# Kernel tuning notes

Hardware: AMD Instinct MI355X
Metric: run time of the kernel (lower is better)

Reference implementation:

```python
import jax, jax.numpy as jnp
import numpy as np

DIM = 512
INNER = 512  # heads*dim_head = 8*64
SCALE = 64 ** -0.5  # dim_head^{-0.5}, applied to BOTH q and k as in the source


def setup_inputs() -> dict:
    key = jax.random.key(0)
    k1, k2, k3, k4 = jax.random.split(key, 4)
    x = jax.random.normal(k1, (8, 2048, DIM), dtype=jnp.float32)
    Wqkv = jax.random.normal(k2, (DIM, 3 * INNER), dtype=jnp.float32) * (DIM ** -0.5)
    Wout = jax.random.normal(k3, (INNER, DIM), dtype=jnp.float32) * (INNER ** -0.5)
    bout = jax.random.normal(k4, (DIM,), dtype=jnp.float32) * 0.01
    return {"x": x, "Wqkv": Wqkv, "Wout": Wout, "bout": bout}


def reference(x, Wqkv, Wout, bout):
    # fused QKV projection (no bias)
    qkv = jnp.einsum("bnd,de->bne", x, Wqkv)
    q, k, v = jnp.split(qkv, 3, axis=-1)
    # note: source scales BOTH q and k by dim_head^{-0.5}
    scores = jnp.einsum("bnd,bmd->bnm", q * SCALE, k * SCALE)  # [B,N,N]
    attn = jax.nn.softmax(scores, axis=-1)
    out = jnp.einsum("bnm,bmd->bnd", attn, v)
    # residual add, then output projection (dropout=0.0 -> identity)
    return jnp.einsum("bnd,de->bne", out + x, Wout) + bout
```

## Files before the change

### kernel.cpp

```cpp
#include <hip/hip_runtime.h>
#include <hip/hip_bf16.h>


typedef __attribute__((ext_vector_type(8))) short bf16x8;
typedef __attribute__((ext_vector_type(4))) float f32x4;

__device__ __forceinline__ unsigned short f2bf(float f) {
  unsigned u = __builtin_bit_cast(unsigned, f);
  u += 0x7fffu + ((u >> 16) & 1u);
  return (unsigned short)(u >> 16);
}
__device__ __forceinline__ float bf2f(unsigned short h) {
  unsigned u = ((unsigned)h) << 16;
  return __builtin_bit_cast(float, u);
}

__device__ __forceinline__ void async16(const unsigned short* g, unsigned short* l) {
  __builtin_amdgcn_global_load_lds(
      (const __attribute__((address_space(1))) unsigned int*)g,
      (__attribute__((address_space(3))) unsigned int*)l, 16, 0, 0);
}

__global__ __launch_bounds__(256) void prep_x(const float* __restrict__ X,
                                              unsigned short* __restrict__ XB) {
  const size_t base = ((size_t)blockIdx.x * 256 + threadIdx.x) * 16;
  f32x4 a0 = *(const f32x4*)&X[base];
  f32x4 a1 = *(const f32x4*)&X[base + 4];
  f32x4 a2 = *(const f32x4*)&X[base + 8];
  f32x4 a3 = *(const f32x4*)&X[base + 12];
  bf16x8 o0, o1;
#pragma unroll
  for (int j = 0; j < 4; ++j) {
    o0[j] = (short)f2bf(a0[j]);
    o0[4 + j] = (short)f2bf(a1[j]);
    o1[j] = (short)f2bf(a2[j]);
    o1[4 + j] = (short)f2bf(a3[j]);
  }
  *(bf16x8*)&XB[base] = o0;
  *(bf16x8*)&XB[base + 8] = o1;
}

__global__ __launch_bounds__(256) void prep_w(const float* __restrict__ W,
                                              unsigned short* __restrict__ WT) {
  const int t = threadIdx.x;
  const int c0 = blockIdx.x * 128 + (t & 15) * 8;
  const int k0 = blockIdx.y * 128 + (t >> 4) * 8;
  float r[8][8];
#pragma unroll
  for (int j = 0; j < 8; ++j) {
    f32x4 lo = *(const f32x4*)&W[(size_t)(k0 + j) * 1536 + c0];
    f32x4 hi = *(const f32x4*)&W[(size_t)(k0 + j) * 1536 + c0 + 4];
#pragma unroll
    for (int q = 0; q < 4; ++q) {
      r[j][q] = lo[q];
      r[j][4 + q] = hi[q];
    }
  }
#pragma unroll
  for (int i = 0; i < 8; ++i) {
    const float scl = (c0 + i < 1024) ? 0.125f : 1.0f;
    bf16x8 o;
#pragma unroll
    for (int j = 0; j < 8; ++j) o[j] = (short)f2bf(r[j][i] * scl);
    *(bf16x8*)&WT[(size_t)(c0 + i) * 512 + k0] = o;
  }
}

__global__ __launch_bounds__(256) void transpose_wout(const float* __restrict__ W,
                                                      unsigned short* __restrict__ WT) {
  const int t = threadIdx.x;
  const int c0 = blockIdx.x * 128 + (t & 15) * 8;
  const int k0 = blockIdx.y * 128 + (t >> 4) * 8;
  float r[8][8];
#pragma unroll
  for (int j = 0; j < 8; ++j) {
    f32x4 lo = *(const f32x4*)&W[(size_t)(k0 + j) * 512 + c0];
    f32x4 hi = *(const f32x4*)&W[(size_t)(k0 + j) * 512 + c0 + 4];
#pragma unroll
    for (int q = 0; q < 4; ++q) {
      r[j][q] = lo[q];
      r[j][4 + q] = hi[q];
    }
  }
#pragma unroll
  for (int i = 0; i < 8; ++i) {
    bf16x8 o;
#pragma unroll
    for (int j = 0; j < 8; ++j) o[j] = (short)f2bf(r[j][i]);
    *(bf16x8*)&WT[(size_t)(c0 + i) * 512 + k0] = o;
  }
}

__global__ __launch_bounds__(256) void transpose_v(const unsigned short* __restrict__ QKV,
                                                   unsigned short* __restrict__ VT) {
  const int t = threadIdx.x;
  const int m0 = blockIdx.x * 128 + (t & 15) * 8;
  const int d0 = blockIdx.y * 128 + (t >> 4) * 8;
  bf16x8 r[8];
#pragma unroll
  for (int j = 0; j < 8; ++j)
    r[j] = *(const bf16x8*)&QKV[(size_t)(m0 + j) * 1536 + 1024 + d0];
#pragma unroll
  for (int i = 0; i < 8; ++i) {
    bf16x8 o;
#pragma unroll
    for (int j = 0; j < 8; ++j) o[j] = r[j][i];
    *(bf16x8*)&VT[(size_t)(d0 + i) * 16384 + m0] = o;
  }
}


#define GEMM97_VARS                                            \
  const int tid = threadIdx.x;                                 \
  const int wave = tid >> 6, lane = tid & 63;                  \
  const int wr = wave >> 1, wc = wave & 1;                     \
  const int lg = lane >> 4, ll = lane & 15;                    \
  const int kk = lg * 8;                                       \
  const int srow = wave * 32 + (lane >> 2);                    \
  const int scol = (lane & 3) * 8;

#define GEMM97_BODY(AG, ASTR, BG, BSTR, KDIM)                                            \
  __shared__ __align__(16) unsigned short Asm[4096];                                     \
  __shared__ __align__(16) unsigned short Bsm[4096];                                     \
  GEMM97_VARS                                                                            \
  f32x4 acc[4][4];                                                                       \
  _Pragma("unroll") for (int i = 0; i < 4; ++i) _Pragma("unroll") for (int j = 0; j < 4; \
                                                                       ++j) acc[i][j] =  \
      (f32x4){0.f, 0.f, 0.f, 0.f};                                                       \
  for (int kt = 0; kt < KDIM; kt += 32) {                                                \
    async16(&AG[(size_t)srow * ASTR + kt + scol], &Asm[wave * 1024]);                    \
    async16(&AG[(size_t)(srow + 16) * ASTR + kt + scol], &Asm[wave * 1024 + 512]);       \
    async16(&BG[(size_t)srow * BSTR + kt + scol], &Bsm[wave * 1024]);                    \
    async16(&BG[(size_t)(srow + 16) * BSTR + kt + scol], &Bsm[wave * 1024 + 512]);       \
    __syncthreads();                                                                     \
    bf16x8 af[4], bfr[4];                                                                \
    _Pragma("unroll") for (int ai = 0; ai < 4; ++ai) af[ai] =                            \
        *(const bf16x8*)&Asm[(wr * 64 + ai * 16 + ll) * 32 + kk];                        \
    _Pragma("unroll") for (int bj = 0; bj < 4; ++bj) bfr[bj] =                           \
        *(const bf16x8*)&Bsm[(wc * 64 + bj * 16 + ll) * 32 + kk];                        \
    _Pragma("unroll") for (int ai = 0; ai < 4; ++ai) _Pragma("unroll") for (int bj = 0;  \
                                                                            bj < 4;      \
                                                                            ++bj)        \
        acc[ai][bj] =                                                                    \
        __builtin_amdgcn_mfma_f32_16x16x32_bf16(af[ai], bfr[bj], acc[ai][bj], 0, 0, 0);  \
    __syncthreads();                                                                     \
  }

__global__ __launch_bounds__(256, 3) void gemm_qkv97(const unsigned short* __restrict__ XB,
                                                     const unsigned short* __restrict__ WT,
                                                     unsigned short* __restrict__ QKV) {
  const int bid = blockIdx.x;
  const int qt = bid / 12, nt = bid - qt * 12;
  const unsigned short* Ag = XB + (size_t)(qt * 128) * 512;
  const unsigned short* Bg = WT + (size_t)(nt * 128) * 512;
  GEMM97_BODY(Ag, 512, Bg, 512, 512)
#pragma unroll
  for (int ai = 0; ai < 4; ++ai)
#pragma unroll
    for (int bj = 0; bj < 4; ++bj) {
      const int col = nt * 128 + wc * 64 + bj * 16 + ll;
#pragma unroll
      for (int r = 0; r < 4; ++r) {
        const int row = qt * 128 + wr * 64 + ai * 16 + lg * 4 + r;
        QKV[(size_t)row * 1536 + col] = f2bf(acc[ai][bj][r]);
      }
    }
}

__global__ __launch_bounds__(256, 3) void sgemm97(const unsigned short* __restrict__ QKV,
                                                  unsigned short* __restrict__ S,
                                                  float* __restrict__ part) {
  const int bid = blockIdx.x;
  const int b = bid & 7;
  const int idx = bid >> 3;
  const int kvt = idx & 15, qt = idx >> 4;
  const unsigned short* Ag = QKV + ((size_t)b * 2048 + qt * 128) * 1536;
  const unsigned short* Bg = QKV + ((size_t)b * 2048 + kvt * 128) * 1536 + 512;
  GEMM97_BODY(Ag, 1536, Bg, 1536, 512)

#pragma unroll
  for (int ai = 0; ai < 4; ++ai)
#pragma unroll
    for (int bj = 0; bj < 4; ++bj)
#pragma unroll
      for (int r = 0; r < 4; ++r) acc[ai][bj][r] = __expf(acc[ai][bj][r]);

#pragma unroll
  for (int ai = 0; ai < 4; ++ai)
#pragma unroll
    for (int r = 0; r < 4; ++r) {
      float se = (acc[ai][0][r] + acc[ai][1][r]) + (acc[ai][2][r] + acc[ai][3][r]);
      se += __shfl_xor(se, 1);
      se += __shfl_xor(se, 2);
      se += __shfl_xor(se, 4);
      se += __shfl_xor(se, 8);
      if (ll == 0) {
        const size_t rowg = (size_t)b * 2048 + qt * 128 + wr * 64 + ai * 16 + lg * 4 + r;
        part[rowg * 32 + kvt * 2 + wc] = se;
      }
    }

  unsigned short* Sg = S + (size_t)b * 2048 * 2048;
#pragma unroll
  for (int ai = 0; ai < 4; ++ai)
#pragma unroll
    for (int bj = 0; bj < 4; ++bj) {
      const int col = kvt * 128 + wc * 64 + bj * 16 + ll;
#pragma unroll
      for (int r = 0; r < 4; ++r) {
        const int row = qt * 128 + wr * 64 + ai * 16 + lg * 4 + r;
        Sg[(size_t)row * 2048 + col] = f2bf(acc[ai][bj][r]);
      }
    }
}

__global__ __launch_bounds__(256) void combine_l(const float* __restrict__ part,
                                                 float* __restrict__ invl) {
  const int row = blockIdx.x * 256 + threadIdx.x;
  float l = 0.f;
#pragma unroll
  for (int t = 0; t < 8; ++t) {
    f32x4 v = *(const f32x4*)&part[(size_t)row * 32 + t * 4];
    l += (v[0] + v[1]) + (v[2] + v[3]);
  }
  invl[row] = 1.0f / l;
}

__global__ __launch_bounds__(256, 3) void pvgemm97(const unsigned short* __restrict__ S,
                                                   const unsigned short* __restrict__ VT,
                                                   const float* __restrict__ X,
                                                   const float* __restrict__ invl,
                                                   unsigned short* __restrict__ RES) {
  __shared__ __align__(16) unsigned short Asm[8192];
  __shared__ __align__(16) unsigned short Bsm[8192];
  const int tid = threadIdx.x;
  const int wave = tid >> 6, lane = tid & 63;
  const int wr = wave >> 1, wc = wave & 1;
  const int lg = lane >> 4, ll = lane & 15;
  const int bid = blockIdx.x;
  const int b = bid & 7;
  const int idx = bid >> 3;
  const int dt = idx & 3, qt = idx >> 2;
  const unsigned short* Ag = S + (size_t)b * 2048 * 2048 + (size_t)(qt * 128) * 2048;
  const unsigned short* Bg = VT + (size_t)(dt * 128) * 16384 + (size_t)b * 2048;
  const int s64row = wave * 32 + (lane >> 3);
  const int s64col = (lane & 7) * 8;

  f32x4 acc[4][4];
#pragma unroll
  for (int i = 0; i < 4; ++i)
#pragma unroll
    for (int j = 0; j < 4; ++j) acc[i][j] = (f32x4){0.f, 0.f, 0.f, 0.f};

  for (int kt = 0; kt < 2048; kt += 64) {
#pragma unroll
    for (int i = 0; i < 4; ++i) {
      async16(&Ag[(size_t)(s64row + i * 8) * 2048 + kt + s64col], &Asm[wave * 2048 + i * 512]);
      async16(&Bg[(size_t)(s64row + i * 8) * 16384 + kt + s64col], &Bsm[wave * 2048 + i * 512]);
    }
    __syncthreads();
#pragma unroll
    for (int half = 0; half < 2; ++half) {
      const int kk64 = half * 32 + lg * 8;
      bf16x8 af[4], bfr[4];
#pragma unroll
      for (int ai = 0; ai < 4; ++ai) af[ai] = *(const bf16x8*)&Asm[(wr * 64 + ai * 16 + ll) * 64 + kk64];
#pragma unroll
      for (int bj = 0; bj < 4; ++bj) bfr[bj] = *(const bf16x8*)&Bsm[(wc * 64 + bj * 16 + ll) * 64 + kk64];
#pragma unroll
      for (int ai = 0; ai < 4; ++ai)
#pragma unroll
        for (int bj = 0; bj < 4; ++bj)
          acc[ai][bj] = __builtin_amdgcn_mfma_f32_16x16x32_bf16(af[ai], bfr[bj], acc[ai][bj], 0, 0, 0);
    }
    __syncthreads();
  }

  const int rowbase = b * 2048 + qt * 128 + wr * 64;
  float il[4][4];
#pragma unroll
  for (int ai = 0; ai < 4; ++ai)
#pragma unroll
    for (int r = 0; r < 4; ++r) il[ai][r] = invl[rowbase + ai * 16 + lg * 4 + r];
#pragma unroll
  for (int ai = 0; ai < 4; ++ai)
#pragma unroll
    for (int bj = 0; bj < 4; ++bj) {
      const int col = dt * 128 + wc * 64 + bj * 16 + ll;
#pragma unroll
      for (int r = 0; r < 4; ++r) {
        const size_t row = (size_t)rowbase + ai * 16 + lg * 4 + r;
        const float val = acc[ai][bj][r] * il[ai][r] + X[row * 512 + col];
        RES[row * 1536 + 1024 + col] = f2bf(val);
      }
    }
}

__global__ __launch_bounds__(256, 3) void gemm_out97(const unsigned short* __restrict__ A,
                                                     const unsigned short* __restrict__ WT,
                                                     const float* __restrict__ bias,
                                                     float* __restrict__ OUT) {
  const int bid = blockIdx.x;
  const int dt = bid & 3, qt = bid >> 2;
  const unsigned short* Ag = A + (size_t)(qt * 128) * 1536 + 1024;
  const unsigned short* Bg = WT + (size_t)(dt * 128) * 512;
  GEMM97_BODY(Ag, 1536, Bg, 512, 512)
#pragma unroll
  for (int ai = 0; ai < 4; ++ai)
#pragma unroll
    for (int bj = 0; bj < 4; ++bj) {
      const int col = dt * 128 + wc * 64 + bj * 16 + ll;
      const float bv = bias[col];
#pragma unroll
      for (int r = 0; r < 4; ++r) {
        const int row = qt * 128 + wr * 64 + ai * 16 + lg * 4 + r;
        OUT[(size_t)row * 512 + col] = acc[ai][bj][r] + bv;
      }
    }
}

extern "C" void kernel_launch(void* const* d_in, const int* in_sizes, int n_in,
                              void* d_out, int out_size, void* d_ws, size_t ws_size,
                              hipStream_t stream) {
  const float* x = (const float*)d_in[0];
  const float* Wqkv = (const float*)d_in[1];
  const float* Wout = (const float*)d_in[2];
  const float* bout = (const float*)d_in[3];
  float* out = (float*)d_out;

  unsigned short* qkvb = (unsigned short*)d_ws;
  unsigned short* VT = qkvb + (size_t)16384 * 1536;
  unsigned short* S = VT + (size_t)512 * 16384;
  unsigned short* xb = S;
  unsigned short* WT = S + (size_t)16384 * 512;
  unsigned short* WoutT = VT;
  float* part = out;
  float* invl = out + (size_t)16384 * 32;

  prep_x<<<2048, 256, 0, stream>>>(x, xb);
  prep_w<<<dim3(12, 4), 256, 0, stream>>>(Wqkv, WT);
  gemm_qkv97<<<1536, 256, 0, stream>>>(xb, WT, qkvb);
  transpose_v<<<dim3(128, 4), 256, 0, stream>>>(qkvb, VT);
  sgemm97<<<2048, 256, 0, stream>>>(qkvb, S, part);
  combine_l<<<64, 256, 0, stream>>>(part, invl);
  pvgemm97<<<512, 256, 0, stream>>>(S, VT, x, invl, qkvb);
  transpose_wout<<<dim3(4, 4), 256, 0, stream>>>(Wout, WoutT);
  gemm_out97<<<512, 256, 0, stream>>>(qkvb, WoutT, bout, out);
}
```

Baseline: 195.0 us.

## Double-buffer LDS in score and PV GEMMs, enlarge score tile to 256x256

The score GEMM moves from 128x128 tiles with 256 threads to 256x256 tiles with 512 threads and double-buffered LDS (64 KB), so the next K slice is prefetched while MFMAs run. The PV GEMM gets the same double-buffering with a single barrier per iteration. Larger tiles cut how often Q and K are re-read from memory. The cost is higher LDS and register use per block, which lowers occupancy, and fewer blocks in the score grid. The partial-sum layout still fills 32 slots per row, which matches what combine_l reads.

```diff
diff --git a/kernel.cpp b/kernel.cpp
--- a/kernel.cpp
+++ b/kernel.cpp
@@ -167,26 +167,73 @@
     }
 }
 
-__global__ __launch_bounds__(256, 3) void sgemm97(const unsigned short* __restrict__ QKV,
-                                                  unsigned short* __restrict__ S,
-                                                  float* __restrict__ part) {
+__global__ __launch_bounds__(512) void sgemm256(const unsigned short* __restrict__ QKV,
+                                                unsigned short* __restrict__ S,
+                                                float* __restrict__ part) {
+  __shared__ __align__(16) unsigned short Asm[2][16384];
+  __shared__ __align__(16) unsigned short Bsm[2][16384];
+  const int tid = threadIdx.x;
+  const int wave = tid >> 6, lane = tid & 63;
+  const int wr = wave >> 2, wc = wave & 3;
+  const int lg = lane >> 4, ll = lane & 15;
   const int bid = blockIdx.x;
   const int b = bid & 7;
   const int idx = bid >> 3;
-  const int kvt = idx & 15, qt = idx >> 4;
-  const unsigned short* Ag = QKV + ((size_t)b * 2048 + qt * 128) * 1536;
-  const unsigned short* Bg = QKV + ((size_t)b * 2048 + kvt * 128) * 1536 + 512;
-  GEMM97_BODY(Ag, 1536, Bg, 1536, 512)
-
-#pragma unroll
-  for (int ai = 0; ai < 4; ++ai)
+  const int kvt = idx & 7, qt = idx >> 3;
+  const unsigned short* Ag = QKV + ((size_t)b * 2048 + qt * 256) * 1536;
+  const unsigned short* Bg = QKV + ((size_t)b * 2048 + kvt * 256) * 1536 + 512;
+  const int sr = wave * 8 + (lane >> 3);
+  const int sc = (lane & 7) * 8;
+
+  f32x4 acc[8][4];
+#pragma unroll
+  for (int i = 0; i < 8; ++i)
+#pragma unroll
+    for (int j = 0; j < 4; ++j) acc[i][j] = (f32x4){0.f, 0.f, 0.f, 0.f};
+
+#define SG_STAGE(BUF, KT)                                                              \
+  _Pragma("unroll") for (int i = 0; i < 4; ++i) {                                      \
+    async16(&Ag[(size_t)(i * 64 + sr) * 1536 + (KT) + sc], &Asm[BUF][(i * 64 + wave * 8) * 64]); \
+    async16(&Bg[(size_t)(i * 64 + sr) * 1536 + (KT) + sc], &Bsm[BUF][(i * 64 + wave * 8) * 64]); \
+  }
+
+  SG_STAGE(0, 0)
+  int cur = 0;
+  __syncthreads();
+  for (int kt = 0; kt < 512; kt += 64) {
+    if (kt + 64 < 512) {
+      if (cur) { SG_STAGE(0, kt + 64) } else { SG_STAGE(1, kt + 64) }
+    }
+#pragma unroll
+    for (int half = 0; half < 2; ++half) {
+      const int kb = half * 32 + lg * 8;
+      bf16x8 af[8], bf4[4];
+#pragma unroll
+      for (int ai = 0; ai < 8; ++ai)
+        af[ai] = *(const bf16x8*)&Asm[cur][(wr * 128 + ai * 16 + ll) * 64 + kb];
+#pragma unroll
+      for (int bj = 0; bj < 4; ++bj)
+        bf4[bj] = *(const bf16x8*)&Bsm[cur][(wc * 64 + bj * 16 + ll) * 64 + kb];
+#pragma unroll
+      for (int ai = 0; ai < 8; ++ai)
+#pragma unroll
+        for (int bj = 0; bj < 4; ++bj)
+          acc[ai][bj] = __builtin_amdgcn_mfma_f32_16x16x32_bf16(af[ai], bf4[bj], acc[ai][bj], 0, 0, 0);
+    }
+    __syncthreads();
+    cur ^= 1;
+  }
+#undef SG_STAGE
+
+#pragma unroll
+  for (int ai = 0; ai < 8; ++ai)
 #pragma unroll
     for (int bj = 0; bj < 4; ++bj)
 #pragma unroll
       for (int r = 0; r < 4; ++r) acc[ai][bj][r] = __expf(acc[ai][bj][r]);
 
 #pragma unroll
-  for (int ai = 0; ai < 4; ++ai)
+  for (int ai = 0; ai < 8; ++ai)
 #pragma unroll
     for (int r = 0; r < 4; ++r) {
       float se = (acc[ai][0][r] + acc[ai][1][r]) + (acc[ai][2][r] + acc[ai][3][r]);
@@ -195,20 +242,20 @@
       se += __shfl_xor(se, 4);
       se += __shfl_xor(se, 8);
       if (ll == 0) {
-        const size_t rowg = (size_t)b * 2048 + qt * 128 + wr * 64 + ai * 16 + lg * 4 + r;
-        part[rowg * 32 + kvt * 2 + wc] = se;
+        const size_t rowg = (size_t)b * 2048 + qt * 256 + wr * 128 + ai * 16 + lg * 4 + r;
+        part[rowg * 32 + kvt * 4 + wc] = se;
       }
     }
 
   unsigned short* Sg = S + (size_t)b * 2048 * 2048;
 #pragma unroll
-  for (int ai = 0; ai < 4; ++ai)
+  for (int ai = 0; ai < 8; ++ai)
 #pragma unroll
     for (int bj = 0; bj < 4; ++bj) {
-      const int col = kvt * 128 + wc * 64 + bj * 16 + ll;
+      const int col = kvt * 256 + wc * 64 + bj * 16 + ll;
 #pragma unroll
       for (int r = 0; r < 4; ++r) {
-        const int row = qt * 128 + wr * 64 + ai * 16 + lg * 4 + r;
+        const int row = qt * 256 + wr * 128 + ai * 16 + lg * 4 + r;
         Sg[(size_t)row * 2048 + col] = f2bf(acc[ai][bj][r]);
       }
     }
@@ -231,8 +278,8 @@
                                                    const float* __restrict__ X,
                                                    const float* __restrict__ invl,
                                                    unsigned short* __restrict__ RES) {
-  __shared__ __align__(16) unsigned short Asm[8192];
-  __shared__ __align__(16) unsigned short Bsm[8192];
+  __shared__ __align__(16) unsigned short Asm[2][8192];
+  __shared__ __align__(16) unsigned short Bsm[2][8192];
   const int tid = threadIdx.x;
   const int wave = tid >> 6, lane = tid & 63;
   const int wr = wave >> 1, wc = wave & 1;
@@ -243,8 +290,8 @@
   const int dt = idx & 3, qt = idx >> 2;
   const unsigned short* Ag = S + (size_t)b * 2048 * 2048 + (size_t)(qt * 128) * 2048;
   const unsigned short* Bg = VT + (size_t)(dt * 128) * 16384 + (size_t)b * 2048;
-  const int s64row = wave * 32 + (lane >> 3);
-  const int s64col = (lane & 7) * 8;
+  const int sr = wave * 32 + (lane >> 3);
+  const int sc = (lane & 7) * 8;
 
   f32x4 acc[4][4];
 #pragma unroll
@@ -252,29 +299,39 @@
 #pragma unroll
     for (int j = 0; j < 4; ++j) acc[i][j] = (f32x4){0.f, 0.f, 0.f, 0.f};
 
+#define PV_STAGE(BUF, KT)                                                                   \
+  _Pragma("unroll") for (int i = 0; i < 4; ++i) {                                           \
+    async16(&Ag[(size_t)(sr + i * 8) * 2048 + (KT) + sc], &Asm[BUF][(wave * 32 + i * 8) * 64]);  \
+    async16(&Bg[(size_t)(sr + i * 8) * 16384 + (KT) + sc], &Bsm[BUF][(wave * 32 + i * 8) * 64]); \
+  }
+
+  PV_STAGE(0, 0)
+  int cur = 0;
+  __syncthreads();
   for (int kt = 0; kt < 2048; kt += 64) {
-#pragma unroll
-    for (int i = 0; i < 4; ++i) {
-      async16(&Ag[(size_t)(s64row + i * 8) * 2048 + kt + s64col], &Asm[wave * 2048 + i * 512]);
-      async16(&Bg[(size_t)(s64row + i * 8) * 16384 + kt + s64col], &Bsm[wave * 2048 + i * 512]);
+    if (kt + 64 < 2048) {
+      if (cur) { PV_STAGE(0, kt + 64) } else { PV_STAGE(1, kt + 64) }
+    }
+#pragma unroll
+    for (int half = 0; half < 2; ++half) {
+      const int kb = half * 32 + lg * 8;
+      bf16x8 af[4], bf4[4];
+#pragma unroll
+      for (int ai = 0; ai < 4; ++ai)
+        af[ai] = *(const bf16x8*)&Asm[cur][(wr * 64 + ai * 16 + ll) * 64 + kb];
+#pragma unroll
+      for (int bj = 0; bj < 4; ++bj)
+        bf4[bj] = *(const bf16x8*)&Bsm[cur][(wc * 64 + bj * 16 + ll) * 64 + kb];
+#pragma unroll
+      for (int ai = 0; ai < 4; ++ai)
+#pragma unroll
+        for (int bj = 0; bj < 4; ++bj)
+          acc[ai][bj] = __builtin_amdgcn_mfma_f32_16x16x32_bf16(af[ai], bf4[bj], acc[ai][bj], 0, 0, 0);
     }
     __syncthreads();
-#pragma unroll
-    for (int half = 0; half < 2; ++half) {
-      const int kk64 = half * 32 + lg * 8;
-      bf16x8 af[4], bfr[4];
-#pragma unroll
-      for (int ai = 0; ai < 4; ++ai) af[ai] = *(const bf16x8*)&Asm[(wr * 64 + ai * 16 + ll) * 64 + kk64];
-#pragma unroll
-      for (int bj = 0; bj < 4; ++bj) bfr[bj] = *(const bf16x8*)&Bsm[(wc * 64 + bj * 16 + ll) * 64 + kk64];
-#pragma unroll
-      for (int ai = 0; ai < 4; ++ai)
-#pragma unroll
-        for (int bj = 0; bj < 4; ++bj)
-          acc[ai][bj] = __builtin_amdgcn_mfma_f32_16x16x32_bf16(af[ai], bfr[bj], acc[ai][bj], 0, 0, 0);
-    }
-    __syncthreads();
-  }
+    cur ^= 1;
+  }
+#undef PV_STAGE
 
   const int rowbase = b * 2048 + qt * 128 + wr * 64;
   float il[4][4];
@@ -341,7 +398,7 @@
   prep_w<<<dim3(12, 4), 256, 0, stream>>>(Wqkv, WT);
   gemm_qkv97<<<1536, 256, 0, stream>>>(xb, WT, qkvb);
   transpose_v<<<dim3(128, 4), 256, 0, stream>>>(qkvb, VT);
-  sgemm97<<<2048, 256, 0, stream>>>(qkvb, S, part);
+  sgemm256<<<512, 512, 0, stream>>>(qkvb, S, part);
   combine_l<<<64, 256, 0, stream>>>(part, invl);
   pvgemm97<<<512, 256, 0, stream>>>(S, VT, x, invl, qkvb);
   transpose_wout<<<dim3(4, 4), 256, 0, stream>>>(Wout, WoutT);
```

Measured after the change: 189.4 us. -2.9%, faster.
